# Kernel optimization log

Hardware: AMD Instinct MI355X
Metric: run time of the kernel (lower is better)

Reference implementation:

```python
import jax, jax.numpy as jnp
import numpy as np
import math

D_MODEL = 1024
NHEAD = 16
HEAD_DIM = D_MODEL // NHEAD
SCALE = math.sqrt(HEAD_DIM)
B, TQ, TK = 8, 1024, 1024


def setup_inputs() -> dict:
    key = jax.random.key(0)
    ks = jax.random.split(key, 8)
    init = 0.02
    return {
        "query": jax.random.normal(ks[0], (B, TQ, D_MODEL), jnp.float32),
        "memory": jax.random.normal(ks[1], (B, TK, D_MODEL), jnp.float32),
        "coverage": jax.random.uniform(ks[2], (B, TK), jnp.float32),
        "Wq": jax.random.normal(ks[3], (D_MODEL, D_MODEL), jnp.float32) * init,
        "bq": jnp.zeros((D_MODEL,), jnp.float32),
        "Wk": jax.random.normal(ks[4], (D_MODEL, D_MODEL), jnp.float32) * init,
        "bk": jnp.zeros((D_MODEL,), jnp.float32),
        "Wv": jax.random.normal(ks[5], (D_MODEL, D_MODEL), jnp.float32) * init,
        "bv": jnp.zeros((D_MODEL,), jnp.float32),
        "Wo": jax.random.normal(ks[6], (D_MODEL, D_MODEL), jnp.float32) * init,
        "bo": jnp.zeros((D_MODEL,), jnp.float32),
        "Wcov": jax.random.normal(ks[7], (NHEAD, 1), jnp.float32) * init,
    }


def reference(query, memory, coverage, Wq, bq, Wk, bk, Wv, bv, Wo, bo, Wcov):
    b, tq, _ = query.shape
    tk = memory.shape[1]
    # projections, split into heads: [B, H, T, hd]
    Q = (query @ Wq.T + bq).reshape(b, tq, NHEAD, HEAD_DIM).transpose(0, 2, 1, 3)
    K = (memory @ Wk.T + bk).reshape(b, tk, NHEAD, HEAD_DIM).transpose(0, 2, 1, 3)
    V = (memory @ Wv.T + bv).reshape(b, tk, NHEAD, HEAD_DIM).transpose(0, 2, 1, 3)
    scores = jnp.einsum('bhqd,bhkd->bhqk', Q, K) / SCALE
    # coverage_proj: Linear(1, nhead, bias=False) -> outer product coverage x Wcov[:,0]
    cov_bias = jnp.einsum('bk,h->bhk', coverage, Wcov[:, 0])[:, :, None, :]  # [B,H,1,Tk]
    scores = scores + cov_bias
    attn = jax.nn.softmax(scores, axis=-1)
    # dropout is identity in eval/deterministic mode
    out = jnp.einsum('bhqk,bhkd->bhqd', attn, V).transpose(0, 2, 1, 3).reshape(b, tq, D_MODEL)
    out = out @ Wo.T + bo
    new_coverage = coverage + attn.mean(axis=1).sum(axis=1)  # [B,Tk]
    return out, new_coverage
```

## Files before the change

### kernel.cpp

```cpp
#include <hip/hip_runtime.h>

typedef __bf16 bf16_t;
typedef bf16_t bf16x8 __attribute__((ext_vector_type(8)));
typedef float f32x4 __attribute__((ext_vector_type(4)));

#define MFMA16(a, b, c) __builtin_amdgcn_mfma_f32_16x16x32_bf16(a, b, c, 0, 0, 0)

#define LOG2E 1.44269504f
#define C1 0.18033688f

__device__ inline void async_copy16(const bf16_t* g, bf16_t* l) {
  __builtin_amdgcn_global_load_lds(
      (const __attribute__((address_space(1))) void*)g,
      (__attribute__((address_space(3))) void*)l, 16, 0, 0);
}

__device__ inline bf16x8 lds_frag(const bf16_t* lds, int row, int c8) {
  return *(const bf16x8*)(lds + row * 64 + ((c8 ^ (row & 7)) << 3));
}

template <int NCHUNK, int NT>
__device__ inline void stage_tile(const bf16_t* __restrict__ g, size_t ld,
                                  bf16_t* lds, int tid) {
#pragma unroll
  for (int it = 0; it < NCHUNK / NT; ++it) {
    int f = it * NT + tid;
    int row = f >> 3;
    int c8 = (f & 7) ^ (row & 7);
    async_copy16(g + (size_t)row * ld + c8 * 8, lds + f * 8);
  }
}

__global__ __launch_bounds__(256) void convert_kernel(
    const float* __restrict__ q, const float* __restrict__ mem,
    const float* __restrict__ wq, const float* __restrict__ wk,
    const float* __restrict__ wv, const float* __restrict__ wo, bf16_t* Xq,
    bf16_t* Xm, bf16_t* Wqb, bf16_t* Wkb, bf16_t* Wvb, bf16_t* Wob) {
  size_t i = ((size_t)blockIdx.x * 256 + threadIdx.x) * 8;
  const float* src;
  bf16_t* dst;
  size_t off;
  if (i < 8388608u)        { src = q;   dst = Xq;  off = i; }
  else if (i < 16777216u)  { src = mem; dst = Xm;  off = i - 8388608u; }
  else if (i < 17825792u)  { src = wq;  dst = Wqb; off = i - 16777216u; }
  else if (i < 18874368u)  { src = wk;  dst = Wkb; off = i - 17825792u; }
  else if (i < 19922944u)  { src = wv;  dst = Wvb; off = i - 18874368u; }
  else                     { src = wo;  dst = Wob; off = i - 19922944u; }
  float4 f0 = *(const float4*)(src + off);
  float4 f1 = *(const float4*)(src + off + 4);
  union { bf16_t h[8]; uint4 u; } t;
  t.h[0] = (bf16_t)f0.x; t.h[1] = (bf16_t)f0.y;
  t.h[2] = (bf16_t)f0.z; t.h[3] = (bf16_t)f0.w;
  t.h[4] = (bf16_t)f1.x; t.h[5] = (bf16_t)f1.y;
  t.h[6] = (bf16_t)f1.z; t.h[7] = (bf16_t)f1.w;
  *(uint4*)(dst + off) = t.u;
}

__global__ __launch_bounds__(256) void gemm_qkv(
    const bf16_t* __restrict__ Xq, const bf16_t* __restrict__ Xm,
    const bf16_t* __restrict__ Wqkv, const float* __restrict__ bq,
    const float* __restrict__ bk, const float* __restrict__ bv,
    bf16_t* __restrict__ Qp, bf16_t* __restrict__ Kp,
    bf16_t* __restrict__ Vt) {
  __shared__ bf16_t As[128 * 64];
  __shared__ bf16_t Bs[128 * 64];
  const int tid = threadIdx.x;
  const int wave = tid >> 6, lane = tid & 63, quad = lane >> 4, c = lane & 15;
  const int wm = (wave & 1) * 64, wn = (wave >> 1) * 64;
  const size_t bm = blockIdx.x, bn = blockIdx.y;
  const int which = (int)(bn >> 3);
  const bf16_t* A = which ? Xm : Xq;
  const float* bias = which == 0 ? bq : (which == 1 ? bk : bv);
  const bf16_t* Ab = A + bm * 128 * 1024;
  const bf16_t* Bb = Wqkv + bn * 128 * 1024;
  const f32x4 z4 = {0.f, 0.f, 0.f, 0.f};
  f32x4 acc[4][4];
#pragma unroll
  for (int i = 0; i < 4; ++i)
#pragma unroll
    for (int j = 0; j < 4; ++j) acc[i][j] = z4;

  for (int kt = 0; kt < 16; ++kt) {
    if (kt) __syncthreads();
    stage_tile<1024, 256>(Ab + kt * 64, 1024, As, tid);
    stage_tile<1024, 256>(Bb + kt * 64, 1024, Bs, tid);
    __syncthreads();
#pragma unroll
    for (int ks = 0; ks < 2; ++ks) {
      bf16x8 af[4], bfr[4];
#pragma unroll
      for (int i = 0; i < 4; ++i)
        af[i] = lds_frag(As, wm + 16 * i + c, ks * 4 + quad);
#pragma unroll
      for (int j = 0; j < 4; ++j)
        bfr[j] = lds_frag(Bs, wn + 16 * j + c, ks * 4 + quad);
#pragma unroll
      for (int i = 0; i < 4; ++i)
#pragma unroll
        for (int j = 0; j < 4; ++j)
          acc[i][j] = MFMA16(af[i], bfr[j], acc[i][j]);
    }
  }
#pragma unroll
  for (int i = 0; i < 4; ++i)
#pragma unroll
    for (int j = 0; j < 4; ++j) {
      int gc = (int)bn * 128 + wn + 16 * j + c;
      int gcl = gc & 1023;
      float bvv = bias[gcl];
      if (which == 2) {
        int b = (int)(bm >> 3);
        int kk = (int)(bm & 7) * 128 + wm + 16 * i + quad * 4;
        union { bf16_t h4[4]; uint2 u; } pk;
#pragma unroll
        for (int r = 0; r < 4; ++r) pk.h4[r] = (bf16_t)(acc[i][j][r] + bvv);
        *(uint2*)(Vt + ((size_t)(b * 1024 + gcl)) * 1024 + kk) = pk.u;
      } else {
        bf16_t* Cout = which ? Kp : Qp;
        int gr0 = (int)bm * 128 + wm + 16 * i + quad * 4;
#pragma unroll
        for (int r = 0; r < 4; ++r)
          Cout[(size_t)(gr0 + r) * 1024 + gcl] = (bf16_t)(acc[i][j][r] + bvv);
      }
    }
}

__global__ __launch_bounds__(256) void gemm_out(
    const bf16_t* __restrict__ A, const bf16_t* __restrict__ Bw,
    const float* __restrict__ bias, float* __restrict__ Cout) {
  __shared__ bf16_t As[128 * 64];
  __shared__ bf16_t Bs[128 * 64];
  const int tid = threadIdx.x;
  const int wave = tid >> 6, lane = tid & 63, quad = lane >> 4, c = lane & 15;
  const int wm = (wave & 1) * 64, wn = (wave >> 1) * 64;
  const size_t bm = blockIdx.x, bn = blockIdx.y;
  const bf16_t* Ab = A + bm * 128 * 1024;
  const bf16_t* Bb = Bw + bn * 128 * 1024;
  const f32x4 z4 = {0.f, 0.f, 0.f, 0.f};
  f32x4 acc[4][4];
#pragma unroll
  for (int i = 0; i < 4; ++i)
#pragma unroll
    for (int j = 0; j < 4; ++j) acc[i][j] = z4;

  for (int kt = 0; kt < 16; ++kt) {
    if (kt) __syncthreads();
    stage_tile<1024, 256>(Ab + kt * 64, 1024, As, tid);
    stage_tile<1024, 256>(Bb + kt * 64, 1024, Bs, tid);
    __syncthreads();
#pragma unroll
    for (int ks = 0; ks < 2; ++ks) {
      bf16x8 af[4], bfr[4];
#pragma unroll
      for (int i = 0; i < 4; ++i)
        af[i] = lds_frag(As, wm + 16 * i + c, ks * 4 + quad);
#pragma unroll
      for (int j = 0; j < 4; ++j)
        bfr[j] = lds_frag(Bs, wn + 16 * j + c, ks * 4 + quad);
#pragma unroll
      for (int i = 0; i < 4; ++i)
#pragma unroll
        for (int j = 0; j < 4; ++j)
          acc[i][j] = MFMA16(af[i], bfr[j], acc[i][j]);
    }
  }
#pragma unroll
  for (int i = 0; i < 4; ++i)
#pragma unroll
    for (int j = 0; j < 4; ++j) {
      int gc = (int)bn * 128 + wn + 16 * j + c;
      float bvv = bias[gc];
      int gr0 = (int)bm * 128 + wm + 16 * i + quad * 4;
#pragma unroll
      for (int r = 0; r < 4; ++r)
        Cout[(size_t)(gr0 + r) * 1024 + gc] = acc[i][j][r] + bvv;
    }
}

__global__ __launch_bounds__(256) void attn_fwd(
    const bf16_t* __restrict__ Qp, const bf16_t* __restrict__ Kp,
    const bf16_t* __restrict__ Vt, const float* __restrict__ coverage,
    const float* __restrict__ Wcov, bf16_t* __restrict__ Hb,
    float* __restrict__ part) {
  __shared__ bf16_t Qs[64 * 64];
  __shared__ bf16_t Ks[64 * 64];
  __shared__ bf16_t Vs[64 * 64];
  __shared__ bf16_t Ps[4][16 * 64];
  __shared__ float covb[1024];
  __shared__ float covsum[1024];
  const int tid = threadIdx.x;
  const int wave = tid >> 6, lane = tid & 63, quad = lane >> 4, c = lane & 15;
  const int qx = blockIdx.x, h = blockIdx.y, b = blockIdx.z;
  const int q0 = qx * 64;
  const float wcl = Wcov[h] * LOG2E;
  const f32x4 z4 = {0.f, 0.f, 0.f, 0.f};

  stage_tile<512, 256>(Qp + ((size_t)(b * 1024 + q0)) * 1024 + h * 64, 1024,
                       Qs, tid);
  for (int i = tid; i < 1024; i += 256) {
    covb[i] = coverage[b * 1024 + i] * wcl;
    covsum[i] = 0.f;
  }

  float lpart = 0.f;
  f32x4 O[4] = {z4, z4, z4, z4};
  bf16x8 qf0, qf1;
  bf16_t* Pw = &Ps[wave][0];

  for (int kt = 0; kt < 16; ++kt) {
    const int k0 = kt * 64;
    if (kt) __syncthreads();
    stage_tile<512, 256>(Kp + ((size_t)(b * 1024 + k0)) * 1024 + h * 64, 1024,
                         Ks, tid);
    stage_tile<512, 256>(Vt + ((size_t)(b * 1024 + h * 64)) * 1024 + k0, 1024,
                         Vs, tid);
    __syncthreads();
    if (kt == 0) {
      qf0 = lds_frag(Qs, wave * 16 + c, quad);
      qf1 = lds_frag(Qs, wave * 16 + c, 4 + quad);
    }
    f32x4 S[4] = {z4, z4, z4, z4};
#pragma unroll
    for (int j = 0; j < 4; ++j) {
      S[j] = MFMA16(lds_frag(Ks, j * 16 + c, quad), qf0, S[j]);
      S[j] = MFMA16(lds_frag(Ks, j * 16 + c, 4 + quad), qf1, S[j]);
    }
#pragma unroll
    for (int j = 0; j < 4; ++j) {
      f32x4 cb = *(const f32x4*)&covb[k0 + j * 16 + quad * 4];
      union { bf16_t h4[4]; uint2 u; } pk;
#pragma unroll
      for (int r = 0; r < 4; ++r) {
        float p = exp2f(S[j][r] * C1 + cb[r]);
        lpart += p;
        pk.h4[r] = (bf16_t)p;
      }
      int k8 = j * 2 + (quad >> 1);
      *(uint2*)(Pw + c * 64 + ((k8 ^ (c & 7)) << 3) + (quad & 1) * 4) = pk.u;
    }
#pragma unroll
    for (int ks = 0; ks < 2; ++ks) {
      bf16x8 pb =
          *(const bf16x8*)(Pw + c * 64 + (((ks * 4 + quad) ^ (c & 7)) << 3));
#pragma unroll
      for (int j = 0; j < 4; ++j)
        O[j] = MFMA16(lds_frag(Vs, j * 16 + c, ks * 4 + quad), pb, O[j]);
    }
  }

  lpart += __shfl_xor(lpart, 16);
  lpart += __shfl_xor(lpart, 32);
  float linv = 1.f / lpart;

  size_t rowbase = ((size_t)(b * 1024 + q0 + wave * 16 + c)) * 1024 + h * 64;
#pragma unroll
  for (int j = 0; j < 4; ++j) {
    union { bf16_t h4[4]; uint2 u; } pk;
#pragma unroll
    for (int r = 0; r < 4; ++r) pk.h4[r] = (bf16_t)(O[j][r] * linv);
    *(uint2*)(Hb + rowbase + j * 16 + quad * 4) = pk.u;
  }

  float linv_r[4];
#pragma unroll
  for (int r = 0; r < 4; ++r) linv_r[r] = __shfl(linv, quad * 4 + r);

  __syncthreads();
  stage_tile<512, 256>(Kp + ((size_t)(b * 1024)) * 1024 + h * 64, 1024, Ks,
                       tid);
  __syncthreads();
  for (int kt = 0; kt < 16; ++kt) {
    const int k0 = kt * 64;
    bf16_t* cur = (kt & 1) ? Vs : Ks;
    if (kt < 15) {
      bf16_t* nxt = (kt & 1) ? Ks : Vs;
      stage_tile<512, 256>(
          Kp + ((size_t)(b * 1024 + k0 + 64)) * 1024 + h * 64, 1024, nxt, tid);
    }
    f32x4 S[4] = {z4, z4, z4, z4};
#pragma unroll
    for (int j = 0; j < 4; ++j) {
      S[j] = MFMA16(qf0, lds_frag(cur, j * 16 + c, quad), S[j]);
      S[j] = MFMA16(qf1, lds_frag(cur, j * 16 + c, 4 + quad), S[j]);
    }
#pragma unroll
    for (int j = 0; j < 4; ++j) {
      float cb = covb[k0 + j * 16 + c];
      float vsum = 0.f;
#pragma unroll
      for (int r = 0; r < 4; ++r)
        vsum += exp2f(S[j][r] * C1 + cb) * linv_r[r];
      vsum += __shfl_xor(vsum, 16);
      vsum += __shfl_xor(vsum, 32);
      if (quad == 0) atomicAdd(&covsum[k0 + j * 16 + c], vsum);
    }
    __syncthreads();
  }
  float* ps = part + ((size_t)(b * 256 + h * 16 + qx)) * 1024;
  for (int i = tid; i < 1024; i += 256) ps[i] = covsum[i];
}

__global__ __launch_bounds__(256) void cov_reduce(
    const float* __restrict__ part, const float* __restrict__ coverage,
    float* __restrict__ covout) {
  int i = blockIdx.x * 256 + threadIdx.x;
  int b = i >> 10, k = i & 1023;
  const float* p = part + (size_t)b * 256 * 1024 + k;
  float s = 0.f;
  for (int j = 0; j < 256; ++j) s += p[(size_t)j * 1024];
  covout[i] = coverage[i] + s * 0.0625f;
}

extern "C" void kernel_launch(void* const* d_in, const int* in_sizes, int n_in,
                              void* d_out, int out_size, void* d_ws,
                              size_t ws_size, hipStream_t stream) {
  const float* query = (const float*)d_in[0];
  const float* memory = (const float*)d_in[1];
  const float* coverage = (const float*)d_in[2];
  const float* Wq = (const float*)d_in[3];
  const float* bq = (const float*)d_in[4];
  const float* Wk = (const float*)d_in[5];
  const float* bk = (const float*)d_in[6];
  const float* Wv = (const float*)d_in[7];
  const float* bv = (const float*)d_in[8];
  const float* Wo = (const float*)d_in[9];
  const float* bo = (const float*)d_in[10];
  const float* Wcov = (const float*)d_in[11];

  char* w = (char*)d_ws;
  const size_t MB = 1024 * 1024;
  bf16_t* Xq = (bf16_t*)(w + 0);
  bf16_t* Xm = (bf16_t*)(w + 16 * MB);
  bf16_t* Wqb = (bf16_t*)(w + 32 * MB);
  bf16_t* Wkb = (bf16_t*)(w + 34 * MB);
  bf16_t* Wvb = (bf16_t*)(w + 36 * MB);
  bf16_t* Wob = (bf16_t*)(w + 38 * MB);
  bf16_t* Qp = (bf16_t*)(w + 40 * MB);
  bf16_t* Kp = (bf16_t*)(w + 56 * MB);
  bf16_t* Vt = (bf16_t*)(w + 72 * MB);
  bf16_t* Hb = (bf16_t*)(w + 0);
  float* part = (float*)(w + 16 * MB);

  float* out = (float*)d_out;
  float* covout = out + (size_t)8 * 1024 * 1024;

  convert_kernel<<<10240, 256, 0, stream>>>(query, memory, Wq, Wk, Wv, Wo, Xq,
                                            Xm, Wqb, Wkb, Wvb, Wob);
  gemm_qkv<<<dim3(64, 24), 256, 0, stream>>>(Xq, Xm, Wqb, bq, bk, bv, Qp, Kp,
                                             Vt);
  attn_fwd<<<dim3(16, 16, 8), 256, 0, stream>>>(Qp, Kp, Vt, coverage, Wcov,
                                                Hb, part);
  gemm_out<<<dim3(64, 8), 256, 0, stream>>>(Hb, Wob, bo, out);
  cov_reduce<<<32, 256, 0, stream>>>(part, coverage, covout);
}
```

Baseline: 355.2 us.

## Double-buffer attention K/V tiles and split coverage sum into separate key-major kernel

The attention kernel now double-buffers K and V tiles in LDS so the next tile is prefetched while the current one is computed, using explicit waitcnt and barriers. The row sum is taken with an extra MFMA against a ones vector instead of a scalar accumulation. The second pass that recomputed scores for the coverage update moves into a new key-major kernel that reads the per-row inverse normalizers from global memory. Its results are added atomically into the coverage output, which the convert kernel now pre-initialises with a copy of coverage. This removes the large partial buffer and the reduction kernel, at the cost of an extra launch and float atomics whose summation order is nondeterministic.

```diff
diff --git a/kernel.cpp b/kernel.cpp
--- a/kernel.cpp
+++ b/kernel.cpp
@@ -8,6 +8,16 @@
 
 #define LOG2E 1.44269504f
 #define C1 0.18033688f
+
+#define WAIT_VM4_LGKM0 0x074
+#define WAIT_VM2_LGKM0 0x072
+#define WAIT_VM0_LGKM0 0x070
+
+__device__ inline void barrier_ws() {
+  __asm__ volatile("" ::: "memory");
+  __builtin_amdgcn_s_barrier();
+  __asm__ volatile("" ::: "memory");
+}
 
 __device__ inline void async_copy16(const bf16_t* g, bf16_t* l) {
   __builtin_amdgcn_global_load_lds(
@@ -34,9 +44,16 @@
 __global__ __launch_bounds__(256) void convert_kernel(
     const float* __restrict__ q, const float* __restrict__ mem,
     const float* __restrict__ wq, const float* __restrict__ wk,
-    const float* __restrict__ wv, const float* __restrict__ wo, bf16_t* Xq,
-    bf16_t* Xm, bf16_t* Wqb, bf16_t* Wkb, bf16_t* Wvb, bf16_t* Wob) {
+    const float* __restrict__ wv, const float* __restrict__ wo,
+    const float* __restrict__ coverage, bf16_t* Xq, bf16_t* Xm, bf16_t* Wqb,
+    bf16_t* Wkb, bf16_t* Wvb, bf16_t* Wob, float* covout) {
   size_t i = ((size_t)blockIdx.x * 256 + threadIdx.x) * 8;
+  if (i >= 20971520u) {
+    size_t off = i - 20971520u;
+    *(float4*)(covout + off) = *(const float4*)(coverage + off);
+    *(float4*)(covout + off + 4) = *(const float4*)(coverage + off + 4);
+    return;
+  }
   const float* src;
   bf16_t* dst;
   size_t off;
@@ -181,60 +198,63 @@
     const bf16_t* __restrict__ Qp, const bf16_t* __restrict__ Kp,
     const bf16_t* __restrict__ Vt, const float* __restrict__ coverage,
     const float* __restrict__ Wcov, bf16_t* __restrict__ Hb,
-    float* __restrict__ part) {
+    float* __restrict__ linvG) {
   __shared__ bf16_t Qs[64 * 64];
-  __shared__ bf16_t Ks[64 * 64];
-  __shared__ bf16_t Vs[64 * 64];
+  __shared__ bf16_t Ks[2][64 * 64];
+  __shared__ bf16_t Vs[2][64 * 64];
   __shared__ bf16_t Ps[4][16 * 64];
   __shared__ float covb[1024];
-  __shared__ float covsum[1024];
   const int tid = threadIdx.x;
   const int wave = tid >> 6, lane = tid & 63, quad = lane >> 4, c = lane & 15;
-  const int qx = blockIdx.x, h = blockIdx.y, b = blockIdx.z;
-  const int q0 = qx * 64;
+  const int q0 = blockIdx.x * 64, h = blockIdx.y, b = blockIdx.z;
   const float wcl = Wcov[h] * LOG2E;
   const f32x4 z4 = {0.f, 0.f, 0.f, 0.f};
+  const bf16_t* Kbase = Kp + ((size_t)b * 1024) * 1024 + h * 64;
+  const bf16_t* Vbase = Vt + ((size_t)(b * 1024 + h * 64)) * 1024;
 
   stage_tile<512, 256>(Qp + ((size_t)(b * 1024 + q0)) * 1024 + h * 64, 1024,
                        Qs, tid);
-  for (int i = tid; i < 1024; i += 256) {
-    covb[i] = coverage[b * 1024 + i] * wcl;
-    covsum[i] = 0.f;
-  }
-
-  float lpart = 0.f;
+  for (int i = tid; i < 1024; i += 256) covb[i] = coverage[b * 1024 + i] * wcl;
+  stage_tile<512, 256>(Kbase, 1024, Ks[0], tid);
+  stage_tile<512, 256>(Vbase, 1024, Vs[0], tid);
+
   f32x4 O[4] = {z4, z4, z4, z4};
+  f32x4 Ol = z4;
   bf16x8 qf0, qf1;
+  union { bf16_t h8[8]; bf16x8 v; } ones;
+#pragma unroll
+  for (int t = 0; t < 8; ++t) ones.h8[t] = (bf16_t)1.0f;
   bf16_t* Pw = &Ps[wave][0];
 
-  for (int kt = 0; kt < 16; ++kt) {
-    const int k0 = kt * 64;
-    if (kt) __syncthreads();
-    stage_tile<512, 256>(Kp + ((size_t)(b * 1024 + k0)) * 1024 + h * 64, 1024,
-                         Ks, tid);
-    stage_tile<512, 256>(Vt + ((size_t)(b * 1024 + h * 64)) * 1024 + k0, 1024,
-                         Vs, tid);
-    __syncthreads();
+  auto tile_step = [&](int kt, const bf16_t* curK, const bf16_t* curV,
+                       bf16_t* nxtK, bf16_t* nxtV) {
+    if (kt < 15) {
+      stage_tile<512, 256>(Kbase + (size_t)(kt + 1) * 64 * 1024, 1024, nxtK,
+                           tid);
+      stage_tile<512, 256>(Vbase + (kt + 1) * 64, 1024, nxtV, tid);
+      __builtin_amdgcn_s_waitcnt(WAIT_VM4_LGKM0);
+    } else {
+      __builtin_amdgcn_s_waitcnt(WAIT_VM0_LGKM0);
+    }
+    barrier_ws();
     if (kt == 0) {
       qf0 = lds_frag(Qs, wave * 16 + c, quad);
       qf1 = lds_frag(Qs, wave * 16 + c, 4 + quad);
     }
+    const int k0 = kt * 64;
     f32x4 S[4] = {z4, z4, z4, z4};
 #pragma unroll
     for (int j = 0; j < 4; ++j) {
-      S[j] = MFMA16(lds_frag(Ks, j * 16 + c, quad), qf0, S[j]);
-      S[j] = MFMA16(lds_frag(Ks, j * 16 + c, 4 + quad), qf1, S[j]);
+      S[j] = MFMA16(lds_frag(curK, j * 16 + c, quad), qf0, S[j]);
+      S[j] = MFMA16(lds_frag(curK, j * 16 + c, 4 + quad), qf1, S[j]);
     }
 #pragma unroll
     for (int j = 0; j < 4; ++j) {
       f32x4 cb = *(const f32x4*)&covb[k0 + j * 16 + quad * 4];
       union { bf16_t h4[4]; uint2 u; } pk;
 #pragma unroll
-      for (int r = 0; r < 4; ++r) {
-        float p = exp2f(S[j][r] * C1 + cb[r]);
-        lpart += p;
-        pk.h4[r] = (bf16_t)p;
-      }
+      for (int r = 0; r < 4; ++r)
+        pk.h4[r] = (bf16_t)exp2f(S[j][r] * C1 + cb[r]);
       int k8 = j * 2 + (quad >> 1);
       *(uint2*)(Pw + c * 64 + ((k8 ^ (c & 7)) << 3) + (quad & 1) * 4) = pk.u;
     }
@@ -244,13 +264,21 @@
           *(const bf16x8*)(Pw + c * 64 + (((ks * 4 + quad) ^ (c & 7)) << 3));
 #pragma unroll
       for (int j = 0; j < 4; ++j)
-        O[j] = MFMA16(lds_frag(Vs, j * 16 + c, ks * 4 + quad), pb, O[j]);
-    }
-  }
-
-  lpart += __shfl_xor(lpart, 16);
-  lpart += __shfl_xor(lpart, 32);
-  float linv = 1.f / lpart;
+        O[j] = MFMA16(lds_frag(curV, j * 16 + c, ks * 4 + quad), pb, O[j]);
+      Ol = MFMA16(ones.v, pb, Ol);
+    }
+    barrier_ws();
+  };
+
+#pragma unroll 1
+  for (int kt2 = 0; kt2 < 16; kt2 += 2) {
+    tile_step(kt2, Ks[0], Vs[0], Ks[1], Vs[1]);
+    tile_step(kt2 + 1, Ks[1], Vs[1], Ks[0], Vs[0]);
+  }
+
+  float linv = 1.f / Ol[0];
+  if (quad == 0)
+    linvG[((size_t)(b * 16 + h)) * 1024 + q0 + wave * 16 + c] = linv;
 
   size_t rowbase = ((size_t)(b * 1024 + q0 + wave * 16 + c)) * 1024 + h * 64;
 #pragma unroll
@@ -260,55 +288,95 @@
     for (int r = 0; r < 4; ++r) pk.h4[r] = (bf16_t)(O[j][r] * linv);
     *(uint2*)(Hb + rowbase + j * 16 + quad * 4) = pk.u;
   }
-
-  float linv_r[4];
-#pragma unroll
-  for (int r = 0; r < 4; ++r) linv_r[r] = __shfl(linv, quad * 4 + r);
-
+}
+
+__global__ __launch_bounds__(256) void cov_kernel(
+    const bf16_t* __restrict__ Qp, const bf16_t* __restrict__ Kp,
+    const float* __restrict__ coverage, const float* __restrict__ Wcov,
+    const float* __restrict__ linvG, float* __restrict__ covout) {
+  __shared__ bf16_t Ks[64 * 64];
+  __shared__ bf16_t Qs[2][64 * 64];
+  __shared__ float covsum[64];
+  const int tid = threadIdx.x;
+  const int wave = tid >> 6, lane = tid & 63, quad = lane >> 4, c = lane & 15;
+  const int k0 = blockIdx.x * 64, h = blockIdx.y, b = blockIdx.z;
+  const float wcl = Wcov[h] * LOG2E;
+  const f32x4 z4 = {0.f, 0.f, 0.f, 0.f};
+  const bf16_t* Qbase = Qp + ((size_t)b * 1024) * 1024 + h * 64;
+  const float* lbase = linvG + ((size_t)(b * 16 + h)) * 1024 + wave * 16 + c;
+
+  f32x4 cbv[4];
+#pragma unroll
+  for (int j = 0; j < 4; ++j) {
+    cbv[j] = *(const f32x4*)&coverage[b * 1024 + k0 + j * 16 + quad * 4];
+#pragma unroll
+    for (int r = 0; r < 4; ++r) cbv[j][r] *= wcl;
+  }
+  float lv_cur = lbase[0];
+
+  if (tid < 64) covsum[tid] = 0.f;
+  stage_tile<512, 256>(Kp + ((size_t)(b * 1024 + k0)) * 1024 + h * 64, 1024,
+                       Ks, tid);
+  stage_tile<512, 256>(Qbase, 1024, Qs[0], tid);
+
+  float cs[4][4] = {};
+  bf16x8 kf0[4], kf1[4];
+
+  auto q_step = [&](int qt, const bf16_t* curQ, bf16_t* nxtQ) {
+    float lv_nxt = 0.f;
+    if (qt < 15) {
+      lv_nxt = lbase[(qt + 1) * 64];
+      stage_tile<512, 256>(Qbase + (size_t)(qt + 1) * 64 * 1024, 1024, nxtQ,
+                           tid);
+      __builtin_amdgcn_s_waitcnt(WAIT_VM2_LGKM0);
+    } else {
+      __builtin_amdgcn_s_waitcnt(WAIT_VM0_LGKM0);
+    }
+    barrier_ws();
+    if (qt == 0) {
+#pragma unroll
+      for (int j = 0; j < 4; ++j) {
+        kf0[j] = lds_frag(Ks, j * 16 + c, quad);
+        kf1[j] = lds_frag(Ks, j * 16 + c, 4 + quad);
+      }
+    }
+    bf16x8 qa = lds_frag(curQ, wave * 16 + c, quad);
+    bf16x8 qb = lds_frag(curQ, wave * 16 + c, 4 + quad);
+    f32x4 S[4] = {z4, z4, z4, z4};
+#pragma unroll
+    for (int j = 0; j < 4; ++j) {
+      S[j] = MFMA16(kf0[j], qa, S[j]);
+      S[j] = MFMA16(kf1[j], qb, S[j]);
+    }
+#pragma unroll
+    for (int j = 0; j < 4; ++j)
+#pragma unroll
+      for (int r = 0; r < 4; ++r)
+        cs[j][r] += exp2f(S[j][r] * C1 + cbv[j][r]) * lv_cur;
+    lv_cur = lv_nxt;
+    barrier_ws();
+  };
+
+#pragma unroll 1
+  for (int qt2 = 0; qt2 < 16; qt2 += 2) {
+    q_step(qt2, Qs[0], Qs[1]);
+    q_step(qt2 + 1, Qs[1], Qs[0]);
+  }
+
+#pragma unroll
+  for (int j = 0; j < 4; ++j)
+#pragma unroll
+    for (int r = 0; r < 4; ++r) {
+      float v = cs[j][r];
+      v += __shfl_xor(v, 1);
+      v += __shfl_xor(v, 2);
+      v += __shfl_xor(v, 4);
+      v += __shfl_xor(v, 8);
+      if (c == 0) atomicAdd(&covsum[j * 16 + quad * 4 + r], v);
+    }
   __syncthreads();
-  stage_tile<512, 256>(Kp + ((size_t)(b * 1024)) * 1024 + h * 64, 1024, Ks,
-                       tid);
-  __syncthreads();
-  for (int kt = 0; kt < 16; ++kt) {
-    const int k0 = kt * 64;
-    bf16_t* cur = (kt & 1) ? Vs : Ks;
-    if (kt < 15) {
-      bf16_t* nxt = (kt & 1) ? Ks : Vs;
-      stage_tile<512, 256>(
-          Kp + ((size_t)(b * 1024 + k0 + 64)) * 1024 + h * 64, 1024, nxt, tid);
-    }
-    f32x4 S[4] = {z4, z4, z4, z4};
-#pragma unroll
-    for (int j = 0; j < 4; ++j) {
-      S[j] = MFMA16(qf0, lds_frag(cur, j * 16 + c, quad), S[j]);
-      S[j] = MFMA16(qf1, lds_frag(cur, j * 16 + c, 4 + quad), S[j]);
-    }
-#pragma unroll
-    for (int j = 0; j < 4; ++j) {
-      float cb = covb[k0 + j * 16 + c];
-      float vsum = 0.f;
-#pragma unroll
-      for (int r = 0; r < 4; ++r)
-        vsum += exp2f(S[j][r] * C1 + cb) * linv_r[r];
-      vsum += __shfl_xor(vsum, 16);
-      vsum += __shfl_xor(vsum, 32);
-      if (quad == 0) atomicAdd(&covsum[k0 + j * 16 + c], vsum);
-    }
-    __syncthreads();
-  }
-  float* ps = part + ((size_t)(b * 256 + h * 16 + qx)) * 1024;
-  for (int i = tid; i < 1024; i += 256) ps[i] = covsum[i];
-}
-
-__global__ __launch_bounds__(256) void cov_reduce(
-    const float* __restrict__ part, const float* __restrict__ coverage,
-    float* __restrict__ covout) {
-  int i = blockIdx.x * 256 + threadIdx.x;
-  int b = i >> 10, k = i & 1023;
-  const float* p = part + (size_t)b * 256 * 1024 + k;
-  float s = 0.f;
-  for (int j = 0; j < 256; ++j) s += p[(size_t)j * 1024];
-  covout[i] = coverage[i] + s * 0.0625f;
+  if (tid < 64)
+    atomicAdd(&covout[b * 1024 + k0 + tid], covsum[tid] * 0.0625f);
 }
 
 extern "C" void kernel_launch(void* const* d_in, const int* in_sizes, int n_in,
@@ -339,17 +407,19 @@
   bf16_t* Kp = (bf16_t*)(w + 56 * MB);
   bf16_t* Vt = (bf16_t*)(w + 72 * MB);
   bf16_t* Hb = (bf16_t*)(w + 0);
-  float* part = (float*)(w + 16 * MB);
+  float* linvG = (float*)(w + 16 * MB);
 
   float* out = (float*)d_out;
   float* covout = out + (size_t)8 * 1024 * 1024;
 
-  convert_kernel<<<10240, 256, 0, stream>>>(query, memory, Wq, Wk, Wv, Wo, Xq,
-                                            Xm, Wqb, Wkb, Wvb, Wob);
+  convert_kernel<<<10244, 256, 0, stream>>>(query, memory, Wq, Wk, Wv, Wo,
+                                            coverage, Xq, Xm, Wqb, Wkb, Wvb,
+                                            Wob, covout);
   gemm_qkv<<<dim3(64, 24), 256, 0, stream>>>(Xq, Xm, Wqb, bq, bk, bv, Qp, Kp,
                                              Vt);
   attn_fwd<<<dim3(16, 16, 8), 256, 0, stream>>>(Qp, Kp, Vt, coverage, Wcov,
-                                                Hb, part);
+                                                Hb, linvG);
+  cov_kernel<<<dim3(16, 16, 8), 256, 0, stream>>>(Qp, Kp, coverage, Wcov,
+                                                  linvG, covout);
   gemm_out<<<dim3(64, 8), 256, 0, stream>>>(Hb, Wob, bo, out);
-  cov_reduce<<<32, 256, 0, stream>>>(part, coverage, covout);
-}
+}
```

Result: faster. 346.2 us (-2.5%).
